# Kernel tuning notes

Measured on AMD Instinct MI355X. Metric: run time of the kernel, lower is better.

The kernel has to match this reference:

```python
import jax, jax.numpy as jnp
import numpy as np

H = 16      # num_heads
D = 1024    # input_dim
F = 4096    # feed_forward_hidden_size
B, S = 8, 4096
EPS = 1e-6


def _ln(x, g, b):
    mu = jnp.mean(x, axis=-1, keepdims=True)
    var = jnp.mean(jnp.square(x - mu), axis=-1, keepdims=True)
    return (x - mu) * jax.lax.rsqrt(var + EPS) * g + b


def _attn(Q, K, V):
    # per-head attention; original scales by sqrt(input_dim), NOT sqrt(head_dim)
    b, sq, d = Q.shape
    sk = K.shape[1]
    dh = d // H
    Qh = Q.reshape(b, sq, H, dh)
    Kh = K.reshape(b, sk, H, dh)
    Vh = V.reshape(b, sk, H, dh)
    scores = jnp.einsum('bqhd,bkhd->bhqk', Qh, Kh) / jnp.sqrt(jnp.float32(d))
    w = jax.nn.softmax(scores, axis=-1)
    return jnp.einsum('bhqk,bkhd->bqhd', w, Vh).reshape(b, sq, d)


def setup_inputs() -> dict:
    key = jax.random.key(0)
    ks = jax.random.split(key, 10)
    sc = 0.02
    np.random.seed(42)
    decode_input = jnp.asarray(np.random.random([B, 1, D]).astype(np.float32))
    return {
        'key': jax.random.normal(ks[0], (B, S, D), jnp.float32),
        'value': jax.random.normal(ks[1], (B, S, D), jnp.float32),
        'decode_input': decode_input,
        'Wq': jax.random.normal(ks[2], (D, D), jnp.float32) * sc,
        'bq': jnp.zeros((D,), jnp.float32),
        'Wk': jax.random.normal(ks[3], (D, D), jnp.float32) * sc,
        'bk': jnp.zeros((D,), jnp.float32),
        'Wv': jax.random.normal(ks[4], (D, D), jnp.float32) * sc,
        'bv': jnp.zeros((D,), jnp.float32),
        'Wo': jax.random.normal(ks[5], (D, D), jnp.float32) * sc,
        'bo': jnp.zeros((D,), jnp.float32),
        'W1': jax.random.normal(ks[6], (D, F), jnp.float32) * sc,
        'b1': jnp.zeros((F,), jnp.float32),
        'W2': jax.random.normal(ks[7], (F, D), jnp.float32) * sc,
        'b2': jnp.zeros((D,), jnp.float32),
        'ln2_g': jnp.ones((D,), jnp.float32),
        'ln2_b': jnp.zeros((D,), jnp.float32),
        'lnf_g': jnp.ones((D,), jnp.float32),
        'lnf_b': jnp.zeros((D,), jnp.float32),
    }


def reference(key, value, decode_input, Wq, bq, Wk, bk, Wv, bv, Wo, bo,
              W1, b1, W2, b2, ln2_g, ln2_b, lnf_g, lnf_b):
    # K/V projections shared by both attention calls (original reuses mha_1)
    K = key @ Wk + bk            # [B,S,D]
    V = value @ Wv + bv          # [B,S,D]

    # mha_1: self-attention of decode_input would use its own K/V, but here
    # q=k=v=decode_input for the first call
    Q1 = decode_input @ Wq + bq
    K1 = decode_input @ Wk + bk
    V1 = decode_input @ Wv + bv
    mha1_out = _attn(Q1, K1, V1) @ Wo + bo   # [B,1,D]
    # note: layer_norm_mha_1 output is computed in original but never used

    # second call (original buggily calls mha_1 again): q=mha1_out (un-normed)
    Q2 = mha1_out @ Wq + bq
    mha2_out = _attn(Q2, K, V) @ Wo + bo     # [B,1,D]
    x = _ln(mha2_out + decode_input, ln2_g, ln2_b)

    ff = jax.nn.relu(x @ W1 + b1) @ W2 + b2
    return _ln(ff + x, lnf_g, lnf_b)
```

## Files before the change

### kernel.cpp

```cpp
#include <hip/hip_runtime.h>
#include <hip/hip_bf16.h>

#define NB 8
#define NS 4096
#define ND 1024
#define NH 16
#define NF 4096

typedef __attribute__((ext_vector_type(8))) short s16x8;
typedef __attribute__((ext_vector_type(4))) float f32x4;

__device__ __forceinline__ short f2bfs(float x) {
    __hip_bfloat16 h = __float2bfloat16(x);
    return *reinterpret_cast<short*>(&h);
}

__device__ __forceinline__ s16x8 pack8(float4 a, float4 b) {
    s16x8 r;
    r[0]=f2bfs(a.x); r[1]=f2bfs(a.y); r[2]=f2bfs(a.z); r[3]=f2bfs(a.w);
    r[4]=f2bfs(b.x); r[5]=f2bfs(b.y); r[6]=f2bfs(b.z); r[7]=f2bfs(b.w);
    return r;
}


template<int KC>
__global__ void __launch_bounds__(256) mvV_k(const float* __restrict__ x,
        const float* __restrict__ W, int K, int Cout, float* __restrict__ Pout)
{
    __shared__ float xs[KC * 8];
    int tid = threadIdx.x;
    int c = blockIdx.x * 256 + tid;
    int k0 = blockIdx.y * KC;
    for (int i = tid; i < KC * 8; i += 256) {
        int k = i >> 3, b = i & 7;
        xs[i] = x[(size_t)b * K + k0 + k];
    }
    __syncthreads();
    const float* Wp = W + (size_t)k0 * Cout + c;
    float acc[8] = {0,0,0,0,0,0,0,0};
    #pragma unroll 16
    for (int k = 0; k < KC; ++k) {
        float wv = Wp[(size_t)k * Cout];
        float4 x0 = *(const float4*)&xs[k * 8];
        float4 x1 = *(const float4*)&xs[k * 8 + 4];
        acc[0] += x0.x * wv; acc[1] += x0.y * wv; acc[2] += x0.z * wv; acc[3] += x0.w * wv;
        acc[4] += x1.x * wv; acc[5] += x1.y * wv; acc[6] += x1.z * wv; acc[7] += x1.w * wv;
    }
    float* op = Pout + ((size_t)blockIdx.y * 8) * Cout + c;
    #pragma unroll
    for (int b = 0; b < 8; ++b) op[(size_t)b * Cout] = acc[b];
}

template<int KC, int NP, int RELU>
__global__ void __launch_bounds__(256) mvP_k(const float* __restrict__ P,
        const float* __restrict__ bias, const float* __restrict__ W,
        int K, int Cout, float* __restrict__ Pout)
{
    __shared__ float xs[KC * 8];
    int tid = threadIdx.x;
    int c = blockIdx.x * 256 + tid;
    int k0 = blockIdx.y * KC;
    for (int i = tid; i < KC * 8; i += 256) {
        int b = i / KC, k = i % KC;
        float t = bias[k0 + k];
        #pragma unroll 8
        for (int p = 0; p < NP; ++p) t += P[((size_t)(p * 8 + b)) * K + k0 + k];
        if (RELU) t = fmaxf(t, 0.f);
        xs[k * 8 + b] = t;
    }
    __syncthreads();
    const float* Wp = W + (size_t)k0 * Cout + c;
    float acc[8] = {0,0,0,0,0,0,0,0};
    #pragma unroll 16
    for (int k = 0; k < KC; ++k) {
        float wv = Wp[(size_t)k * Cout];
        float4 x0 = *(const float4*)&xs[k * 8];
        float4 x1 = *(const float4*)&xs[k * 8 + 4];
        acc[0] += x0.x * wv; acc[1] += x0.y * wv; acc[2] += x0.z * wv; acc[3] += x0.w * wv;
        acc[4] += x1.x * wv; acc[5] += x1.y * wv; acc[6] += x1.z * wv; acc[7] += x1.w * wv;
    }
    float* op = Pout + ((size_t)blockIdx.y * 8) * Cout + c;
    #pragma unroll
    for (int b = 0; b < 8; ++b) op[(size_t)b * Cout] = acc[b];
}

__global__ void __launch_bounds__(256) u_k(const float* __restrict__ P,
        const float* __restrict__ bq, const float* __restrict__ Wk,
        unsigned short* __restrict__ u16)
{
    int bh = blockIdx.x;
    int b = bh >> 4, h = bh & 15;
    int lane = threadIdx.x & 63, wv = threadIdx.x >> 6;
    int cc = h * 64 + lane;
    float q = bq[cc];
    #pragma unroll 8
    for (int p = 0; p < 64; ++p) q += P[((size_t)(p * 8 + b)) * 1024 + cc];
    int dbase = blockIdx.y * 256;
    #pragma unroll 4
    for (int d = dbase + wv; d < dbase + 256; d += 4) {
        float v = Wk[(size_t)d * 1024 + cc] * q;
        for (int off = 32; off; off >>= 1) v += __shfl_down(v, off);
        if (lane == 0) u16[(size_t)bh * 1024 + d] = (unsigned short)f2bfs(v);
    }
}

__global__ void __launch_bounds__(256) lnp_k(const float* __restrict__ P, int np,
        const float* __restrict__ bias, const float* __restrict__ add,
        const float* __restrict__ g, const float* __restrict__ be,
        float* __restrict__ out)
{
    int b = blockIdx.x, tid = threadIdx.x;
    __shared__ float sd[4];
    int c = tid * 4;
    f32x4 t = *(const f32x4*)&bias[c];
    t += *(const f32x4*)&add[(size_t)b * 1024 + c];
    #pragma unroll 8
    for (int p = 0; p < np; ++p)
        t += *(const f32x4*)&P[((size_t)(p * 8 + b)) * 1024 + c];
    float loc = t[0] + t[1] + t[2] + t[3];
    for (int off = 32; off; off >>= 1) loc += __shfl_down(loc, off);
    if ((tid & 63) == 0) sd[tid >> 6] = loc;
    __syncthreads();
    float mu = (sd[0] + sd[1] + sd[2] + sd[3]) * (1.f / 1024.f);
    __syncthreads();
    f32x4 d = t - mu;
    float v = d[0]*d[0] + d[1]*d[1] + d[2]*d[2] + d[3]*d[3];
    for (int off = 32; off; off >>= 1) v += __shfl_down(v, off);
    if ((tid & 63) == 0) sd[tid >> 6] = v;
    __syncthreads();
    float var = (sd[0] + sd[1] + sd[2] + sd[3]) * (1.f / 1024.f);
    float rs = rsqrtf(var + 1e-6f);
    f32x4 gg = *(const f32x4*)&g[c];
    f32x4 bb = *(const f32x4*)&be[c];
    f32x4 o = d * rs * gg + bb;
    *(f32x4*)&out[(size_t)b * 1024 + c] = o;
}

__global__ void __launch_bounds__(256) scoresx_k(const float* __restrict__ key,
        const unsigned short* __restrict__ u16, float* __restrict__ wexp,
        float* __restrict__ dnm)
{
    __shared__ __align__(16) unsigned short ul[16][1032];
    __shared__ float pls[16][64];
    int b = blockIdx.x, ch = blockIdx.y, tid = threadIdx.x;
    int s0 = ch * 64;
    const uint4* src = (const uint4*)(u16 + (size_t)b * NH * 1024);
    for (int v = tid; v < 2048; v += 256) {
        int h = v >> 7, col = (v & 127) * 8;
        *(uint4*)&ul[h][col] = src[v];
    }
    __syncthreads();
    int lane = tid & 63, wv = tid >> 6;
    int r = lane & 15, g = lane >> 4;
    const float* kp0 = key + ((size_t)(b * NS + s0 + wv * 16 + r)) * ND + g * 8;
    f32x4 acc = {0.f, 0.f, 0.f, 0.f};
    float4 c0,c1,c2,c3,c4,c5,c6,c7, n0,n1,n2,n3,n4,n5,n6,n7;
    c0 = *(const float4*)(kp0);       c1 = *(const float4*)(kp0 + 4);
    c2 = *(const float4*)(kp0 + 32);  c3 = *(const float4*)(kp0 + 36);
    c4 = *(const float4*)(kp0 + 64);  c5 = *(const float4*)(kp0 + 68);
    c6 = *(const float4*)(kp0 + 96);  c7 = *(const float4*)(kp0 + 100);
    #pragma unroll
    for (int k = 0; k < 1024; k += 128) {
        if (k + 128 < 1024) {
            const float* p = kp0 + k + 128;
            n0 = *(const float4*)(p);       n1 = *(const float4*)(p + 4);
            n2 = *(const float4*)(p + 32);  n3 = *(const float4*)(p + 36);
            n4 = *(const float4*)(p + 64);  n5 = *(const float4*)(p + 68);
            n6 = *(const float4*)(p + 96);  n7 = *(const float4*)(p + 100);
        }
        s16x8 a0 = *(const s16x8*)&ul[r][k + g * 8];
        acc = __builtin_amdgcn_mfma_f32_16x16x32_bf16(a0, pack8(c0, c1), acc, 0, 0, 0);
        s16x8 a1 = *(const s16x8*)&ul[r][k + 32 + g * 8];
        acc = __builtin_amdgcn_mfma_f32_16x16x32_bf16(a1, pack8(c2, c3), acc, 0, 0, 0);
        s16x8 a2 = *(const s16x8*)&ul[r][k + 64 + g * 8];
        acc = __builtin_amdgcn_mfma_f32_16x16x32_bf16(a2, pack8(c4, c5), acc, 0, 0, 0);
        s16x8 a3 = *(const s16x8*)&ul[r][k + 96 + g * 8];
        acc = __builtin_amdgcn_mfma_f32_16x16x32_bf16(a3, pack8(c6, c7), acc, 0, 0, 0);
        c0 = n0; c1 = n1; c2 = n2; c3 = n3;
        c4 = n4; c5 = n5; c6 = n6; c7 = n7;
    }
    const float scl = 1.f / 32.f;
    #pragma unroll
    for (int j = 0; j < 4; ++j) {
        int h = g * 4 + j;
        float e = __expf(acc[j] * scl);
        wexp[((size_t)(b * NH + h)) * NS + s0 + wv * 16 + r] = e;
        pls[h][wv * 16 + r] = e;
    }
    __syncthreads();
    if (tid < 16) {
        float s = 0.f;
        #pragma unroll 16
        for (int si = 0; si < 64; ++si) s += pls[tid][si];
        dnm[((size_t)(ch * 8 + b)) * 16 + tid] = s;
    }
}

__global__ void __launch_bounds__(256, 4) poolx_k(const float* __restrict__ value,
        const float* __restrict__ wexp, float* __restrict__ plp)
{
    __shared__ float pl[16][64];
    __shared__ f32x4 red[16][128];
    int b = blockIdx.x, ch = blockIdx.y, dh = blockIdx.z, tid = threadIdx.x;
    int s0 = ch * 64;
    {
        int h = tid >> 4, col = (tid & 15) * 4;
        *(f32x4*)&pl[h][col] = *(const f32x4*)&wexp[((size_t)(b * NH + h)) * NS + s0 + col];
    }
    __syncthreads();
    int dt = tid & 127, sg = tid >> 7;
    const float* vp = value + ((size_t)(b * NS + s0 + sg * 32)) * ND + dh * 512 + dt * 4;
    f32x4 acc[16];
    #pragma unroll
    for (int h = 0; h < 16; ++h) acc[h] = (f32x4){0.f, 0.f, 0.f, 0.f};
    f32x4 v0, v1, v2, v3;
    v0 = *(const f32x4*)(vp + 0*ND); v1 = *(const f32x4*)(vp + 1*ND);
    v2 = *(const f32x4*)(vp + 2*ND); v3 = *(const f32x4*)(vp + 3*ND);
    for (int g = 0; g < 32; g += 4) {
        f32x4 n0, n1, n2, n3;
        if (g + 4 < 32) {
            const float* p = vp + (size_t)(g + 4) * ND;
            n0 = *(const f32x4*)(p + 0*ND); n1 = *(const f32x4*)(p + 1*ND);
            n2 = *(const f32x4*)(p + 2*ND); n3 = *(const f32x4*)(p + 3*ND);
        }
        #pragma unroll
        for (int h = 0; h < 16; ++h) {
            f32x4 wa = *(const f32x4*)&pl[h][sg * 32 + g];
            acc[h] += v0 * wa[0] + v1 * wa[1] + v2 * wa[2] + v3 * wa[3];
        }
        v0 = n0; v1 = n1; v2 = n2; v3 = n3;
    }
    if (sg == 1) {
        #pragma unroll
        for (int h = 0; h < 16; ++h) red[h][dt] = acc[h];
    }
    __syncthreads();
    if (sg == 0) {
        float* o = plp + ((size_t)((ch * 8 + b) * 16)) * 1024 + dh * 512 + dt * 4;
        #pragma unroll
        for (int h = 0; h < 16; ++h)
            *(f32x4*)(o + (size_t)h * 1024) = acc[h] + red[h][dt];
    }
}

template<int KC, int NCH>
__global__ void __launch_bounds__(256) mvH_k(const float* __restrict__ plp,
        const float* __restrict__ dnm, const float* __restrict__ W,
        float* __restrict__ Pout)
{
    __shared__ float xs[4 * KC * 8];
    int tid = threadIdx.x, lane = tid & 63, wv = tid >> 6;
    int c = blockIdx.x * 256 + tid;
    int k0 = blockIdx.y * KC;
    int h = blockIdx.x * 4 + wv;
    float den = 0.f;
    if (lane < 8) {
        #pragma unroll 8
        for (int ch = 0; ch < NCH; ++ch)
            den += dnm[((size_t)(ch * 8 + lane)) * 16 + h];
    }
    float inv8 = (lane < 8) ? 1.f / den : 0.f;
    for (int i = lane; i < 8 * KC; i += 64) {
        int b = i / KC, k = i % KC;
        float t = 0.f;
        #pragma unroll 8
        for (int ch = 0; ch < NCH; ++ch)
            t += plp[((size_t)((ch * 8 + b) * 16 + h)) * 1024 + k0 + k];
        xs[wv * 8 * KC + k * 8 + b] = t * __shfl(inv8, b);
    }
    __syncthreads();
    const float* Wp = W + (size_t)k0 * 1024 + c;
    float acc[8] = {0,0,0,0,0,0,0,0};
    #pragma unroll 16
    for (int k = 0; k < KC; ++k) {
        float wvv = Wp[(size_t)k * 1024];
        float4 x0 = *(const float4*)&xs[wv * 8 * KC + k * 8];
        float4 x1 = *(const float4*)&xs[wv * 8 * KC + k * 8 + 4];
        acc[0] += x0.x * wvv; acc[1] += x0.y * wvv; acc[2] += x0.z * wvv; acc[3] += x0.w * wvv;
        acc[4] += x1.x * wvv; acc[5] += x1.y * wvv; acc[6] += x1.z * wvv; acc[7] += x1.w * wvv;
    }
    float* op = Pout + ((size_t)blockIdx.y * 8) * 1024 + c;
    #pragma unroll
    for (int b = 0; b < 8; ++b) op[(size_t)b * 1024] = acc[b];
}

extern "C" void kernel_launch(void* const* d_in, const int* in_sizes, int n_in,
                              void* d_out, int out_size, void* d_ws, size_t ws_size,
                              hipStream_t stream)
{
    const float* key   = (const float*)d_in[0];
    const float* value = (const float*)d_in[1];
    const float* dec   = (const float*)d_in[2];
    const float* Wq = (const float*)d_in[3];  const float* bq = (const float*)d_in[4];
    const float* Wk = (const float*)d_in[5];
    const float* Wv = (const float*)d_in[7];  const float* bv = (const float*)d_in[8];
    const float* Wo = (const float*)d_in[9];  const float* bo = (const float*)d_in[10];
    const float* W1 = (const float*)d_in[11]; const float* b1 = (const float*)d_in[12];
    const float* W2 = (const float*)d_in[13]; const float* b2 = (const float*)d_in[14];
    const float* g2 = (const float*)d_in[15]; const float* be2 = (const float*)d_in[16];
    const float* gf = (const float*)d_in[17]; const float* bef = (const float*)d_in[18];

    float* ws = (float*)d_ws;
    float* Pa   = ws;
    float* Pb   = Pa   + 524288;
    float* Pq   = Pb   + 524288;
    float* wexp = Pq   + 524288;
    float* plp  = wexp + 524288;
    float* dnm  = plp  + 8388608;
    float* Pd   = dnm  + 8192;
    float* Pe   = Pd   + 524288;
    float* Pff1 = Pe   + 524288;
    float* Pff2 = Pff1 + 524288;
    float* xbuf = Pff2 + 524288;
    unsigned short* u16 = (unsigned short*)(xbuf + 8192);
    float* outp = (float*)d_out;

    dim3 blk(256);

    mvV_k<16><<<dim3(4,64), blk, 0, stream>>>(dec, Wv, 1024, 1024, Pa);
    mvP_k<16,64,0><<<dim3(4,64), blk, 0, stream>>>(Pa, bv, Wo, 1024, 1024, Pb);
    mvP_k<16,64,0><<<dim3(4,64), blk, 0, stream>>>(Pb, bo, Wq, 1024, 1024, Pq);
    u_k<<<dim3(128,4), blk, 0, stream>>>(Pq, bq, Wk, u16);

    scoresx_k<<<dim3(8,64), blk, 0, stream>>>(key, u16, wexp, dnm);
    poolx_k<<<dim3(8,64,2), blk, 0, stream>>>(value, wexp, plp);

    mvH_k<16,64><<<dim3(4,64), blk, 0, stream>>>(plp, dnm, Wv, Pd);
    mvP_k<16,64,0><<<dim3(4,64), blk, 0, stream>>>(Pd, bv, Wo, 1024, 1024, Pe);
    lnp_k<<<dim3(8), blk, 0, stream>>>(Pe, 64, bo, dec, g2, be2, xbuf);

    mvV_k<64><<<dim3(16,16), blk, 0, stream>>>(xbuf, W1, 1024, 4096, Pff1);
    mvP_k<64,16,1><<<dim3(4,64), blk, 0, stream>>>(Pff1, b1, W2, 4096, 1024, Pff2);
    lnp_k<<<dim3(8), blk, 0, stream>>>(Pff2, 64, b2, xbuf, gf, bef, outp);

    (void)in_sizes; (void)n_in; (void)out_size; (void)ws_size;
}
```

Measured before the change: 179.0 us.

## Split score kernel over key halves and move exp/denominator into pool kernel

The scores kernel is split along the 1024-wide reduction dimension into two halves (grid z=2), doubling block count. It also reads the bf16 query vectors directly from global memory instead of staging them in LDS. It writes raw partial scores, and the pool kernel now sums the two partials, applies the scale and exp, and computes the per-chunk softmax denominators. This buys more parallelism for the key-streaming pass, at the cost of an extra partial-score buffer, extra reads in the pool kernel, and dropping the pool kernel's occupancy hint in launch_bounds.

After: 182.5 us. About the same (+2.0%).

```diff
diff --git a/kernel.cpp b/kernel.cpp
--- a/kernel.cpp
+++ b/kernel.cpp
@@ -136,78 +136,69 @@
     *(f32x4*)&out[(size_t)b * 1024 + c] = o;
 }
 
-__global__ void __launch_bounds__(256) scoresx_k(const float* __restrict__ key,
-        const unsigned short* __restrict__ u16, float* __restrict__ wexp,
-        float* __restrict__ dnm)
-{
-    __shared__ __align__(16) unsigned short ul[16][1032];
-    __shared__ float pls[16][64];
-    int b = blockIdx.x, ch = blockIdx.y, tid = threadIdx.x;
-    int s0 = ch * 64;
-    const uint4* src = (const uint4*)(u16 + (size_t)b * NH * 1024);
-    for (int v = tid; v < 2048; v += 256) {
-        int h = v >> 7, col = (v & 127) * 8;
-        *(uint4*)&ul[h][col] = src[v];
-    }
-    __syncthreads();
+__global__ void __launch_bounds__(256) scoresy_k(const float* __restrict__ key,
+        const unsigned short* __restrict__ u16, float* __restrict__ scp)
+{
+    int bb = blockIdx.x, ch = blockIdx.y, kh = blockIdx.z;
+    int tid = threadIdx.x;
     int lane = tid & 63, wv = tid >> 6;
     int r = lane & 15, g = lane >> 4;
-    const float* kp0 = key + ((size_t)(b * NS + s0 + wv * 16 + r)) * ND + g * 8;
+    int srow = ch * 64 + wv * 16 + r;
+    const float* kp0 = key + ((size_t)(bb * NS + srow)) * ND + kh * 512 + g * 8;
+    const unsigned short* up = u16 + ((size_t)(bb * 16 + r)) * 1024 + kh * 512 + g * 8;
     f32x4 acc = {0.f, 0.f, 0.f, 0.f};
-    float4 c0,c1,c2,c3,c4,c5,c6,c7, n0,n1,n2,n3,n4,n5,n6,n7;
-    c0 = *(const float4*)(kp0);       c1 = *(const float4*)(kp0 + 4);
-    c2 = *(const float4*)(kp0 + 32);  c3 = *(const float4*)(kp0 + 36);
-    c4 = *(const float4*)(kp0 + 64);  c5 = *(const float4*)(kp0 + 68);
-    c6 = *(const float4*)(kp0 + 96);  c7 = *(const float4*)(kp0 + 100);
-    #pragma unroll
-    for (int k = 0; k < 1024; k += 128) {
-        if (k + 128 < 1024) {
-            const float* p = kp0 + k + 128;
-            n0 = *(const float4*)(p);       n1 = *(const float4*)(p + 4);
-            n2 = *(const float4*)(p + 32);  n3 = *(const float4*)(p + 36);
-            n4 = *(const float4*)(p + 64);  n5 = *(const float4*)(p + 68);
-            n6 = *(const float4*)(p + 96);  n7 = *(const float4*)(p + 100);
+    float4 c0, c1, c2, c3, n0, n1, n2, n3;
+    s16x8 a0, a1, an0, an1;
+    c0 = *(const float4*)(kp0);      c1 = *(const float4*)(kp0 + 4);
+    c2 = *(const float4*)(kp0 + 32); c3 = *(const float4*)(kp0 + 36);
+    a0 = *(const s16x8*)(up);
+    a1 = *(const s16x8*)(up + 32);
+    #pragma unroll
+    for (int k = 0; k < 512; k += 64) {
+        if (k + 64 < 512) {
+            const float* p = kp0 + k + 64;
+            n0 = *(const float4*)(p);      n1 = *(const float4*)(p + 4);
+            n2 = *(const float4*)(p + 32); n3 = *(const float4*)(p + 36);
+            an0 = *(const s16x8*)(up + k + 64);
+            an1 = *(const s16x8*)(up + k + 96);
         }
-        s16x8 a0 = *(const s16x8*)&ul[r][k + g * 8];
         acc = __builtin_amdgcn_mfma_f32_16x16x32_bf16(a0, pack8(c0, c1), acc, 0, 0, 0);
-        s16x8 a1 = *(const s16x8*)&ul[r][k + 32 + g * 8];
         acc = __builtin_amdgcn_mfma_f32_16x16x32_bf16(a1, pack8(c2, c3), acc, 0, 0, 0);
-        s16x8 a2 = *(const s16x8*)&ul[r][k + 64 + g * 8];
-        acc = __builtin_amdgcn_mfma_f32_16x16x32_bf16(a2, pack8(c4, c5), acc, 0, 0, 0);
-        s16x8 a3 = *(const s16x8*)&ul[r][k + 96 + g * 8];
-        acc = __builtin_amdgcn_mfma_f32_16x16x32_bf16(a3, pack8(c6, c7), acc, 0, 0, 0);
         c0 = n0; c1 = n1; c2 = n2; c3 = n3;
-        c4 = n4; c5 = n5; c6 = n6; c7 = n7;
-    }
-    const float scl = 1.f / 32.f;
+        a0 = an0; a1 = an1;
+    }
     #pragma unroll
     for (int j = 0; j < 4; ++j) {
         int h = g * 4 + j;
-        float e = __expf(acc[j] * scl);
-        wexp[((size_t)(b * NH + h)) * NS + s0 + wv * 16 + r] = e;
-        pls[h][wv * 16 + r] = e;
-    }
-    __syncthreads();
-    if (tid < 16) {
-        float s = 0.f;
-        #pragma unroll 16
-        for (int si = 0; si < 64; ++si) s += pls[tid][si];
-        dnm[((size_t)(ch * 8 + b)) * 16 + tid] = s;
-    }
-}
-
-__global__ void __launch_bounds__(256, 4) poolx_k(const float* __restrict__ value,
-        const float* __restrict__ wexp, float* __restrict__ plp)
+        scp[((size_t)((kh * 8 + bb) * 16 + h)) * NS + srow] = acc[j];
+    }
+}
+
+__global__ void __launch_bounds__(256) pooly_k(const float* __restrict__ value,
+        const float* __restrict__ scp, float* __restrict__ plp,
+        float* __restrict__ dnm)
 {
     __shared__ float pl[16][64];
     __shared__ f32x4 red[16][128];
     int b = blockIdx.x, ch = blockIdx.y, dh = blockIdx.z, tid = threadIdx.x;
     int s0 = ch * 64;
     {
-        int h = tid >> 4, col = (tid & 15) * 4;
-        *(f32x4*)&pl[h][col] = *(const f32x4*)&wexp[((size_t)(b * NH + h)) * NS + s0 + col];
-    }
-    __syncthreads();
+        int h = tid >> 4, si4 = (tid & 15) * 4;
+        f32x4 sa = *(const f32x4*)&scp[((size_t)((0 * 8 + b) * 16 + h)) * NS + s0 + si4]
+                 + *(const f32x4*)&scp[((size_t)((1 * 8 + b) * 16 + h)) * NS + s0 + si4];
+        const float scl = 1.f / 32.f;
+        f32x4 e;
+        e[0] = __expf(sa[0] * scl); e[1] = __expf(sa[1] * scl);
+        e[2] = __expf(sa[2] * scl); e[3] = __expf(sa[3] * scl);
+        *(f32x4*)&pl[h][si4] = e;
+    }
+    __syncthreads();
+    if (dh == 0 && tid < 16) {
+        float s = 0.f;
+        #pragma unroll 16
+        for (int si = 0; si < 64; ++si) s += pl[tid][si];
+        dnm[((size_t)(ch * 8 + b)) * 16 + tid] = s;
+    }
     int dt = tid & 127, sg = tid >> 7;
     const float* vp = value + ((size_t)(b * NS + s0 + sg * 32)) * ND + dh * 512 + dt * 4;
     f32x4 acc[16];
@@ -304,8 +295,8 @@
     float* Pa   = ws;
     float* Pb   = Pa   + 524288;
     float* Pq   = Pb   + 524288;
-    float* wexp = Pq   + 524288;
-    float* plp  = wexp + 524288;
+    float* scp  = Pq   + 524288;
+    float* plp  = scp  + 1048576;
     float* dnm  = plp  + 8388608;
     float* Pd   = dnm  + 8192;
     float* Pe   = Pd   + 524288;
@@ -322,8 +313,8 @@
     mvP_k<16,64,0><<<dim3(4,64), blk, 0, stream>>>(Pb, bo, Wq, 1024, 1024, Pq);
     u_k<<<dim3(128,4), blk, 0, stream>>>(Pq, bq, Wk, u16);
 
-    scoresx_k<<<dim3(8,64), blk, 0, stream>>>(key, u16, wexp, dnm);
-    poolx_k<<<dim3(8,64,2), blk, 0, stream>>>(value, wexp, plp);
+    scoresy_k<<<dim3(8,64,2), blk, 0, stream>>>(key, u16, scp);
+    pooly_k<<<dim3(8,64,2), blk, 0, stream>>>(value, scp, plp, dnm);
 
     mvH_k<16,64><<<dim3(4,64), blk, 0, stream>>>(plp, dnm, Wv, Pd);
     mvP_k<16,64,0><<<dim3(4,64), blk, 0, stream>>>(Pd, bv, Wo, 1024, 1024, Pe);
```
